# Kernel optimization log

Hardware: AMD Instinct MI355X
Metric: run time of the kernel (lower is better)

The kernel has to match this reference:

```python
import jax, jax.numpy as jnp
import numpy as np

N_NODES = 100000
N_EDGES = 1600000
IN_DIM, HID_DIM, OUT_DIM = 128, 256, 128


def gcn_conv(x, edge_index, W, b):
    """PyG GCNConv: add self-loops, sym-normalize, linear transform, scatter-add, bias."""
    n = x.shape[0]
    loop = jnp.arange(n, dtype=edge_index.dtype)
    src = jnp.concatenate([edge_index[0], loop])  # message source (x_j)
    dst = jnp.concatenate([edge_index[1], loop])  # aggregation target
    deg = jax.ops.segment_sum(jnp.ones_like(dst, dtype=x.dtype), dst, num_segments=n)
    dinv = jnp.where(deg > 0, deg ** -0.5, 0.0).astype(x.dtype)
    norm = dinv[src] * dinv[dst]                  # [E+N]
    h = x @ W                                     # [N, out]
    msg = h[src] * norm[:, None]                  # [E+N, out] gather
    out = jax.ops.segment_sum(msg, dst, num_segments=n)  # scatter-add
    return out + b


def setup_inputs() -> dict:
    key = jax.random.key(0)
    k = jax.random.split(key, 6)
    x = jax.random.normal(k[0], (N_NODES, IN_DIM), dtype=jnp.float32)
    edge_index = jax.random.randint(k[1], (2, N_EDGES), 0, N_NODES, dtype=jnp.int64)
    # Glorot-ish init for weights
    W1 = jax.random.normal(k[2], (IN_DIM, HID_DIM), dtype=jnp.float32) * (1.0 / np.sqrt(IN_DIM))
    b1 = jnp.zeros((HID_DIM,), dtype=jnp.float32)
    W2 = jax.random.normal(k[3], (HID_DIM, OUT_DIM), dtype=jnp.float32) * (1.0 / np.sqrt(HID_DIM))
    b2 = jnp.zeros((OUT_DIM,), dtype=jnp.float32)
    return {"x": x, "edge_index": edge_index, "W1": W1, "b1": b1, "W2": W2, "b2": b2}


def reference(x, edge_index, W1, b1, W2, b2):
    h = gcn_conv(x, edge_index, W1, b1)
    h = jax.nn.relu(h)  # relu between layers (drop_rate=0 -> no dropout)
    h = gcn_conv(h, edge_index, W2, b2)
    return h
```

## Files before the change

kernel.cpp:

```cpp
#include <hip/hip_runtime.h>
#include <hip/hip_bf16.h>

#define N_NODES 100000
#define N_EDGES 1600000
#define IN_DIM 128
#define HID_DIM 256
#define OUT_DIM 128
#define NB ((N_NODES + 1023) / 1024)
#define DCHUNK 12500
#define EGRID 8192
#define CAP 64
#define NSTRIP (N_NODES / 16)
#define GWAVES 2048

#define PB_ZERO 391
#define PB_E32  3125
#define PB_PREP 258
#define PB_CONVX 12500
#define PB_TOTAL (PB_ZERO + PB_E32 + PB_PREP + PB_CONVX)

typedef __attribute__((ext_vector_type(8))) short bf16x8;
typedef __attribute__((ext_vector_type(4))) float f32x4;
typedef __attribute__((ext_vector_type(4))) float float4v;
typedef unsigned long long ull;
typedef unsigned short u16;

__device__ __forceinline__ float bf2f(u16 u) {
  union { unsigned int i; float f; } c; c.i = ((unsigned int)u) << 16; return c.f;
}
__device__ __forceinline__ u16 f2bf(float f) {
  __hip_bfloat16 h = __float2bfloat16(f);
  return *(u16*)&h;
}

__global__ void detect_kernel(const int* __restrict__ ei,
                              const unsigned int* __restrict__ xw,
                              int* __restrict__ flags) {
  int lane = threadIdx.x;
  const long long* p = (const long long*)ei;
  long long v = p[lane & 15];
  int ebad = (lane < 16) && (v < 0 || v >= N_NODES);
  ull ebm = __ballot(ebad);
  int isf32 = 0;
  #pragma unroll
  for (int i = 0; i < 4; ++i) {
    unsigned int ex = (xw[lane * 4 + i] >> 7) & 0xFF;
    if (ex >= 0xC0) isf32 = 1;
  }
  ull fbm = __ballot(isf32);
  if (lane == 0) {
    flags[0] = (ebm == 0) ? 1 : 0;
    flags[1] = (fbm != 0) ? 1 : 0;
  }
}

__global__ void prologue_kernel(const int* __restrict__ ei, const void* __restrict__ x,
                                const void* __restrict__ W1, const void* __restrict__ b1,
                                const void* __restrict__ W2, const void* __restrict__ b2,
                                const int* __restrict__ flags,
                                int* __restrict__ deg, int* __restrict__ e32,
                                u16* __restrict__ Wt1, u16* __restrict__ Wt2,
                                u16* __restrict__ b1c, u16* __restrict__ b2c,
                                u16* __restrict__ xc) {
  int b = blockIdx.x, tid = threadIdx.x;
  if (b < PB_ZERO) {
    int i = b * 256 + tid;
    if (i < N_NODES) deg[i] = 0;
  } else if (b < PB_ZERO + PB_E32) {
    int i = (b - PB_ZERO) * 256 + tid;
    if (flags[0]) {
      const longlong2* p = (const longlong2*)ei;
      longlong2 v0 = p[i * 2], v1 = p[i * 2 + 1];
      ((int4*)e32)[i] = make_int4((int)v0.x, (int)v0.y, (int)v1.x, (int)v1.y);
    } else {
      ((int4*)e32)[i] = ((const int4*)ei)[i];
    }
  } else if (b < PB_ZERO + PB_E32 + PB_PREP) {
    int i = (b - PB_ZERO - PB_E32) * 256 + tid;
    int f = flags[1];
    auto cvt = [&](const void* P, int idx) -> u16 {
      return f ? f2bf(((const float*)P)[idx]) : ((const u16*)P)[idx];
    };
    if (i < 32768) {
      int k = i >> 8, n = i & 255;
      Wt1[n * 128 + k] = cvt(W1, i);
    } else if (i < 65536) {
      int j = i - 32768;
      int k = j >> 7, n = j & 127;
      Wt2[n * 256 + k] = cvt(W2, j);
    } else if (i < 65792) {
      b1c[i - 65536] = cvt(b1, i - 65536);
    } else if (i < 65920) {
      b2c[i - 65792] = cvt(b2, i - 65792);
    }
  } else {
    int i = (b - PB_ZERO - PB_E32 - PB_PREP) * 256 + tid;
    if (i >= N_NODES * IN_DIM / 4) return;
    if (flags[1]) {
      float4v v = ((const float4v*)x)[i];
      ull w = (ull)f2bf(v.x) | ((ull)f2bf(v.y) << 16) | ((ull)f2bf(v.z) << 32) |
              ((ull)f2bf(v.w) << 48);
      ((ull*)xc)[i] = w;
    } else {
      ((ull*)xc)[i] = ((const ull*)x)[i];
    }
  }
}

__global__ void fill_fixed_kernel(const int* __restrict__ esrc,
                                  const int* __restrict__ edst,
                                  int* __restrict__ cnt, int* __restrict__ csrf) {
  int g = blockIdx.x & 7;
  unsigned lo = (unsigned)(g * DCHUNK);
  unsigned hi = lo + DCHUNK; if (hi > N_NODES) hi = N_NODES;
  int stride = (EGRID >> 3) * 256;
  for (int e = (blockIdx.x >> 3) * 256 + threadIdx.x; e < N_EDGES; e += stride) {
    unsigned d = (unsigned)edst[e];
    if (d >= lo && d < hi) {
      int s = esrc[e];
      int p = atomicAdd(&cnt[d], 1);
      if (p < CAP) csrf[d * CAP + p] = s;
    }
  }
}

__global__ void degnorm_kernel(const int* __restrict__ cnt, float* __restrict__ dinv) {
  int i = blockIdx.x * 256 + threadIdx.x;
  if (i < N_NODES) dinv[i] = rsqrtf((float)(cnt[i] + 1));
}

__global__ void count_kernel(const int* __restrict__ edst, int* __restrict__ deg) {
  int g = blockIdx.x & 7;
  unsigned lo = (unsigned)(g * DCHUNK);
  unsigned hi = lo + DCHUNK; if (hi > N_NODES) hi = N_NODES;
  int stride = (EGRID >> 3) * 256;
  for (int e = (blockIdx.x >> 3) * 256 + threadIdx.x; e < N_EDGES; e += stride) {
    unsigned d = (unsigned)edst[e];
    if (d >= lo && d < hi) atomicAdd(&deg[d], 1);
  }
}

__global__ __launch_bounds__(1024) void bsum_kernel(const int* __restrict__ deg,
                                                    int* __restrict__ bsum, int n) {
  __shared__ int ws[16];
  int tid = threadIdx.x, lane = tid & 63, wid = tid >> 6;
  int idx = blockIdx.x * 1024 + tid;
  int v = (idx < n) ? deg[idx] : 0;
  #pragma unroll
  for (int o = 32; o > 0; o >>= 1) v += __shfl_down(v, o);
  if (lane == 0) ws[wid] = v;
  __syncthreads();
  if (tid == 0) {
    int r = 0;
    #pragma unroll
    for (int i = 0; i < 16; ++i) r += ws[i];
    bsum[blockIdx.x] = r;
  }
}

__global__ void bscan_kernel(const int* __restrict__ bsum, int* __restrict__ boff,
                             int* __restrict__ total, int nb) {
  int lane = threadIdx.x;
  int carry = 0;
  for (int c = 0; c < (nb + 63) / 64; ++c) {
    int idx = c * 64 + lane;
    int v = (idx < nb) ? bsum[idx] : 0;
    int x = v;
    #pragma unroll
    for (int o = 1; o < 64; o <<= 1) {
      int y = __shfl_up(x, o);
      if (lane >= o) x += y;
    }
    if (idx < nb) boff[idx] = carry + x - v;
    carry += __shfl(x, 63);
  }
  if (lane == 0) *total = carry;
}

__global__ __launch_bounds__(1024) void bfill_kernel(const int* __restrict__ deg,
                                                     const int* __restrict__ boff,
                                                     int* __restrict__ off,
                                                     int* __restrict__ cur,
                                                     float* __restrict__ dinv, int n) {
  __shared__ int wsum[16];
  __shared__ int wpre[16];
  int tid = threadIdx.x, lane = tid & 63, wid = tid >> 6;
  int idx = blockIdx.x * 1024 + tid;
  int v = (idx < n) ? deg[idx] : 0;
  int x = v;
  #pragma unroll
  for (int o = 1; o < 64; o <<= 1) {
    int y = __shfl_up(x, o);
    if (lane >= o) x += y;
  }
  if (lane == 63) wsum[wid] = x;
  __syncthreads();
  if (tid == 0) {
    int r = 0;
    #pragma unroll
    for (int i = 0; i < 16; ++i) { wpre[i] = r; r += wsum[i]; }
  }
  __syncthreads();
  int excl = boff[blockIdx.x] + wpre[wid] + x - v;
  if (idx < n) {
    off[idx] = excl;
    cur[idx] = excl;
    dinv[idx] = rsqrtf((float)(v + 1));
  }
}

__global__ void fill_kernel(const int* __restrict__ esrc, const int* __restrict__ edst,
                            int* __restrict__ cur, int* __restrict__ csr) {
  int g = blockIdx.x & 7;
  unsigned lo = (unsigned)(g * DCHUNK);
  unsigned hi = lo + DCHUNK; if (hi > N_NODES) hi = N_NODES;
  int stride = (EGRID >> 3) * 256;
  for (int e = (blockIdx.x >> 3) * 256 + threadIdx.x; e < N_EDGES; e += stride) {
    unsigned d = (unsigned)edst[e];
    if (d >= lo && d < hi) {
      int s = esrc[e];
      int p = atomicAdd(&cur[d], 1);
      if ((unsigned)p < N_EDGES) csr[p] = s;
    }
  }
}

template <bool BIAS, bool OUTF32, bool FIXED>
__global__ __launch_bounds__(256) void agg_kernel(
    const u16* __restrict__ V, const int* __restrict__ off,
    const int* __restrict__ csr, const float* __restrict__ dinv,
    const u16* __restrict__ bias, void* __restrict__ outv) {
  int d = (blockIdx.x * 256 + threadIdx.x) >> 6;
  int lane = threadIdx.x & 63;
  if (d >= N_NODES) return;
  int du = __builtin_amdgcn_readfirstlane(d);
  int grp = lane >> 4, sub = lane & 15;
  float dv = dinv[du];
  bf16x8 w0 = *(const bf16x8*)(V + (size_t)du * 128 + sub * 8);
  float self_s = (grp == 0) ? dv : 0.0f;
  float a[8];
  #pragma unroll
  for (int k = 0; k < 8; ++k) a[k] = self_s * bf2f((u16)w0[k]);
  int e, e1;
  if (FIXED) {
    int c = __builtin_amdgcn_readfirstlane(off[du]);
    if (c > CAP) c = CAP;
    e = du * CAP;
    e1 = e + c;
  } else {
    e  = __builtin_amdgcn_readfirstlane(off[du]);
    e1 = __builtin_amdgcn_readfirstlane(off[du + 1]);
  }
  for (; e + 8 <= e1; e += 8) {
    int sA = csr[e + grp];
    int sB = csr[e + 4 + grp];
    float dsA = dinv[sA];
    float dsB = dinv[sB];
    bf16x8 wA = *(const bf16x8*)(V + (size_t)sA * 128 + sub * 8);
    bf16x8 wB = *(const bf16x8*)(V + (size_t)sB * 128 + sub * 8);
    #pragma unroll
    for (int k = 0; k < 8; ++k) a[k] = fmaf(dsA, bf2f((u16)wA[k]), a[k]);
    #pragma unroll
    for (int k = 0; k < 8; ++k) a[k] = fmaf(dsB, bf2f((u16)wB[k]), a[k]);
  }
  for (; e + 4 <= e1; e += 4) {
    int s = csr[e + grp];
    float ds = dinv[s];
    bf16x8 w = *(const bf16x8*)(V + (size_t)s * 128 + sub * 8);
    #pragma unroll
    for (int k = 0; k < 8; ++k) a[k] = fmaf(ds, bf2f((u16)w[k]), a[k]);
  }
  int rem = e1 - e;
  if (rem > 0) {
    int ee = e + (grp < rem ? grp : 0);
    int s = csr[ee];
    float ds = (grp < rem) ? dinv[s] : 0.0f;
    bf16x8 w = *(const bf16x8*)(V + (size_t)s * 128 + sub * 8);
    #pragma unroll
    for (int k = 0; k < 8; ++k) a[k] = fmaf(ds, bf2f((u16)w[k]), a[k]);
  }
  #pragma unroll
  for (int k = 0; k < 8; ++k) {
    a[k] += __shfl_xor(a[k], 16);
    a[k] += __shfl_xor(a[k], 32);
    a[k] *= dv;
  }
  if (BIAS) {
    bf16x8 bv = *(const bf16x8*)(bias + sub * 8);
    #pragma unroll
    for (int k = 0; k < 8; ++k) a[k] += bf2f((u16)bv[k]);
  }
  if (OUTF32) {
    if (grp < 2) {
      f32x4 o4;
      #pragma unroll
      for (int r = 0; r < 4; ++r) o4[r] = a[grp * 4 + r];
      *(f32x4*)((float*)outv + (size_t)du * 128 + sub * 8 + grp * 4) = o4;
    }
  } else {
    if (grp == 0) {
      bf16x8 ob;
      #pragma unroll
      for (int k = 0; k < 8; ++k) ob[k] = (short)f2bf(a[k]);
      *(bf16x8*)((u16*)outv + (size_t)du * 128 + sub * 8) = ob;
    }
  }
}

__global__ __launch_bounds__(256) void mlp1_kernel(
    const u16* __restrict__ xa, const u16* __restrict__ Wt1,
    const u16* __restrict__ b1, u16* __restrict__ h) {
  __shared__ u16 B[32768];
  int tid = threadIdx.x;
  #pragma unroll
  for (int j = 0; j < 16; ++j) {
    int i = j * 256 + tid;
    int row = i >> 4, blk = i & 15;
    int phys = (row << 4) | (blk ^ (row & 15));
    *(bf16x8*)&B[phys * 8] = *(const bf16x8*)(Wt1 + (size_t)i * 8);
  }
  __syncthreads();
  int wid = tid >> 6, lane = tid & 63, ml = lane & 15, q = lane >> 4;
  for (int s = blockIdx.x * 4 + wid; s < NSTRIP; s += GWAVES) {
    const short* Ar = (const short*)xa + (size_t)(s * 16 + ml) * IN_DIM + q * 8;
    f32x4 acc[16] = {};
    #pragma unroll
    for (int k0 = 0; k0 < IN_DIM; k0 += 32) {
      bf16x8 a = *(const bf16x8*)(Ar + k0);
      int kb = k0 >> 3;
      #pragma unroll
      for (int t = 0; t < 16; ++t) {
        int brow = t * 16 + ml;
        const u16* Bp = &B[(((unsigned)brow << 4) | (unsigned)((kb + q) ^ ml)) * 8];
        acc[t] = __builtin_amdgcn_mfma_f32_16x16x32_bf16(a, *(const bf16x8*)Bp, acc[t], 0, 0, 0);
      }
    }
    size_t hb = (size_t)s * 16 * HID_DIM;
    #pragma unroll
    for (int t = 0; t < 16; ++t) {
      float bv = bf2f(b1[t * 16 + ml]);
      #pragma unroll
      for (int r = 0; r < 4; ++r)
        h[hb + (size_t)(q * 4 + r) * HID_DIM + t * 16 + ml] =
            f2bf(fmaxf(acc[t][r] + bv, 0.0f));
    }
  }
}

__global__ __launch_bounds__(256) void mlp2_kernel(
    const u16* __restrict__ h, const u16* __restrict__ Wt2, u16* __restrict__ xg) {
  __shared__ u16 B[32768];
  int tid = threadIdx.x;
  #pragma unroll
  for (int j = 0; j < 16; ++j) {
    int i = j * 256 + tid;
    int row = i >> 5, blk = i & 31;
    int phys = (row << 5) | (blk ^ (row & 15));
    *(bf16x8*)&B[phys * 8] = *(const bf16x8*)(Wt2 + (size_t)i * 8);
  }
  __syncthreads();
  int wid = tid >> 6, lane = tid & 63, ml = lane & 15, q = lane >> 4;
  for (int s = blockIdx.x * 4 + wid; s < NSTRIP; s += GWAVES) {
    const short* Ar = (const short*)h + (size_t)(s * 16 + ml) * HID_DIM + q * 8;
    f32x4 acc[8] = {};
    #pragma unroll
    for (int k0 = 0; k0 < HID_DIM; k0 += 32) {
      bf16x8 a = *(const bf16x8*)(Ar + k0);
      int kb = k0 >> 3;
      #pragma unroll
      for (int t = 0; t < 8; ++t) {
        int brow = t * 16 + ml;
        const u16* Bp = &B[(((unsigned)brow << 5) | (unsigned)((kb + q) ^ ml)) * 8];
        acc[t] = __builtin_amdgcn_mfma_f32_16x16x32_bf16(a, *(const bf16x8*)Bp, acc[t], 0, 0, 0);
      }
    }
    size_t gb = (size_t)s * 16 * OUT_DIM;
    #pragma unroll
    for (int t = 0; t < 8; ++t) {
      #pragma unroll
      for (int r = 0; r < 4; ++r)
        xg[gb + (size_t)(q * 4 + r) * OUT_DIM + t * 16 + ml] = f2bf(acc[t][r]);
    }
  }
}

extern "C" void kernel_launch(void* const* d_in, const int* in_sizes, int n_in,
                              void* d_out, int out_size, void* d_ws, size_t ws_size,
                              hipStream_t stream) {
  const void* x  = d_in[0];
  const int*  ei = (const int*)d_in[1];
  const void* W1 = d_in[2];
  const void* b1 = d_in[3];
  const void* W2 = d_in[4];
  const void* b2 = d_in[5];

  char* wsb = (char*)d_ws;

  {
    size_t o = 0;
    auto carve = [&](size_t bytes) {
      o = (o + 511) & ~(size_t)511;
      void* p = wsb + o;
      o += bytes;
      return p;
    };
    int*   flags = (int*)carve(8);
    int*   cnt  = (int*)carve((size_t)N_NODES * 4);
    float* dinv = (float*)carve((size_t)N_NODES * 4);
    int*   csrf = (int*)carve((size_t)N_NODES * CAP * 4);
    u16*   Wt1 = (u16*)carve((size_t)IN_DIM * HID_DIM * 2);
    u16*   Wt2 = (u16*)carve((size_t)HID_DIM * OUT_DIM * 2);
    u16*   b1c = (u16*)carve((size_t)HID_DIM * 2);
    u16*   b2c = (u16*)carve((size_t)OUT_DIM * 2);
    u16*   xc  = (u16*)carve((size_t)N_NODES * 128 * 2);
    u16*   xa  = (u16*)carve((size_t)N_NODES * 128 * 2);
    u16*   h   = (u16*)d_out;
    int*   e32 = (int*)xa;
    int*   esrc = e32;
    int*   edst = e32 + N_EDGES;
    if (o <= ws_size) {
      detect_kernel<<<1, 64, 0, stream>>>(ei, (const unsigned int*)x, flags);
      prologue_kernel<<<PB_TOTAL, 256, 0, stream>>>(ei, x, W1, b1, W2, b2, flags,
                                                    cnt, e32, Wt1, Wt2, b1c, b2c, xc);
      fill_fixed_kernel<<<EGRID, 256, 0, stream>>>(esrc, edst, cnt, csrf);
      degnorm_kernel<<<(N_NODES + 255) / 256, 256, 0, stream>>>(cnt, dinv);
      agg_kernel<false, false, true>
          <<<(N_NODES * 64) / 256, 256, 0, stream>>>(xc, cnt, csrf, dinv, nullptr, xa);
      mlp1_kernel<<<512, 256, 0, stream>>>(xa, Wt1, b1c, h);
      mlp2_kernel<<<512, 256, 0, stream>>>(h, Wt2, xa);
      agg_kernel<true, true, true>
          <<<(N_NODES * 64) / 256, 256, 0, stream>>>(xa, cnt, csrf, dinv, b2c, d_out);
      return;
    }
  }

  size_t o = 0;
  auto carve = [&](size_t bytes) {
    o = (o + 511) & ~(size_t)511;
    void* p = wsb + o;
    o += bytes;
    return p;
  };
  int*   flags = (int*)carve(8);
  int*   deg  = (int*)carve((size_t)N_NODES * 4);
  int*   off  = (int*)carve((size_t)(N_NODES + 1) * 4);
  int*   cur  = (int*)carve((size_t)N_NODES * 4);
  float* dinv = (float*)carve((size_t)N_NODES * 4);
  int*   csr  = (int*)carve((size_t)N_EDGES * 4);
  int*   bsum = (int*)carve((size_t)NB * 4);
  int*   boff = (int*)carve((size_t)NB * 4);
  u16*   Wt1 = (u16*)carve((size_t)IN_DIM * HID_DIM * 2);
  u16*   Wt2 = (u16*)carve((size_t)HID_DIM * OUT_DIM * 2);
  u16*   b1c = (u16*)carve((size_t)HID_DIM * 2);
  u16*   b2c = (u16*)carve((size_t)OUT_DIM * 2);
  u16*   xc  = (u16*)carve((size_t)N_NODES * 128 * 2);
  u16*   xa  = (u16*)carve((size_t)N_NODES * 128 * 2);
  u16*   h   = (u16*)d_out;
  int*   e32 = (int*)xa;
  int*   esrc = e32;
  int*   edst = e32 + N_EDGES;

  detect_kernel<<<1, 64, 0, stream>>>(ei, (const unsigned int*)x, flags);
  prologue_kernel<<<PB_TOTAL, 256, 0, stream>>>(ei, x, W1, b1, W2, b2, flags,
                                                deg, e32, Wt1, Wt2, b1c, b2c, xc);
  count_kernel<<<EGRID, 256, 0, stream>>>(edst, deg);
  bsum_kernel<<<NB, 1024, 0, stream>>>(deg, bsum, N_NODES);
  bscan_kernel<<<1, 64, 0, stream>>>(bsum, boff, off + N_NODES, NB);
  bfill_kernel<<<NB, 1024, 0, stream>>>(deg, boff, off, cur, dinv, N_NODES);
  fill_kernel<<<EGRID, 256, 0, stream>>>(esrc, edst, cur, csr);

  agg_kernel<false, false, false>
      <<<(N_NODES * 64) / 256, 256, 0, stream>>>(xc, off, csr, dinv, nullptr, xa);
  mlp1_kernel<<<512, 256, 0, stream>>>(xa, Wt1, b1c, h);
  mlp2_kernel<<<512, 256, 0, stream>>>(h, Wt2, xa);
  agg_kernel<true, true, false>
      <<<(N_NODES * 64) / 256, 256, 0, stream>>>(xa, off, csr, dinv, b2c, d_out);
}
```

Before: 357.0 us.

## Read int64 edge indices directly in fill kernels, drop int32 conversion pass

Removes the prologue stage that narrowed the int64 edge_index into a temporary int32 buffer; the count, fill and fixed-capacity fill kernels now read the original edge array directly, choosing the dtype at runtime. The fixed-capacity fill is also rewritten so each thread handles 8 consecutive edges with vector loads and one pass over all destinations, replacing the 8-way destination-range partitioned grid-stride loop that rescanned the edge list eight times. This cuts one full write and read of the edge list and most of the redundant destination reads. In exchange, the atomics now hit all destinations at once and lose the locality the range partitioning gave.

```diff
diff --git a/kernel.cpp b/kernel.cpp
--- a/kernel.cpp
+++ b/kernel.cpp
@@ -10,14 +10,14 @@
 #define DCHUNK 12500
 #define EGRID 8192
 #define CAP 64
+#define FFGRID 782
 #define NSTRIP (N_NODES / 16)
 #define GWAVES 2048
 
 #define PB_ZERO 391
-#define PB_E32  3125
 #define PB_PREP 258
 #define PB_CONVX 12500
-#define PB_TOTAL (PB_ZERO + PB_E32 + PB_PREP + PB_CONVX)
+#define PB_TOTAL (PB_ZERO + PB_PREP + PB_CONVX)
 
 typedef __attribute__((ext_vector_type(8))) short bf16x8;
 typedef __attribute__((ext_vector_type(4))) float f32x4;
@@ -54,29 +54,24 @@
   }
 }
 
-__global__ void prologue_kernel(const int* __restrict__ ei, const void* __restrict__ x,
+__device__ __forceinline__ int edge_at(const int* ei, int idx, int mode) {
+  return mode ? (int)((const long long*)ei)[idx] : ei[idx];
+}
+
+__global__ void prologue_kernel(const void* __restrict__ x,
                                 const void* __restrict__ W1, const void* __restrict__ b1,
                                 const void* __restrict__ W2, const void* __restrict__ b2,
                                 const int* __restrict__ flags,
-                                int* __restrict__ deg, int* __restrict__ e32,
+                                int* __restrict__ cnt,
                                 u16* __restrict__ Wt1, u16* __restrict__ Wt2,
                                 u16* __restrict__ b1c, u16* __restrict__ b2c,
                                 u16* __restrict__ xc) {
   int b = blockIdx.x, tid = threadIdx.x;
   if (b < PB_ZERO) {
     int i = b * 256 + tid;
-    if (i < N_NODES) deg[i] = 0;
-  } else if (b < PB_ZERO + PB_E32) {
+    if (i < N_NODES) cnt[i] = 0;
+  } else if (b < PB_ZERO + PB_PREP) {
     int i = (b - PB_ZERO) * 256 + tid;
-    if (flags[0]) {
-      const longlong2* p = (const longlong2*)ei;
-      longlong2 v0 = p[i * 2], v1 = p[i * 2 + 1];
-      ((int4*)e32)[i] = make_int4((int)v0.x, (int)v0.y, (int)v1.x, (int)v1.y);
-    } else {
-      ((int4*)e32)[i] = ((const int4*)ei)[i];
-    }
-  } else if (b < PB_ZERO + PB_E32 + PB_PREP) {
-    int i = (b - PB_ZERO - PB_E32) * 256 + tid;
     int f = flags[1];
     auto cvt = [&](const void* P, int idx) -> u16 {
       return f ? f2bf(((const float*)P)[idx]) : ((const u16*)P)[idx];
@@ -94,7 +89,7 @@
       b2c[i - 65792] = cvt(b2, i - 65792);
     }
   } else {
-    int i = (b - PB_ZERO - PB_E32 - PB_PREP) * 256 + tid;
+    int i = (b - PB_ZERO - PB_PREP) * 256 + tid;
     if (i >= N_NODES * IN_DIM / 4) return;
     if (flags[1]) {
       float4v v = ((const float4v*)x)[i];
@@ -107,37 +102,61 @@
   }
 }
 
-__global__ void fill_fixed_kernel(const int* __restrict__ esrc,
-                                  const int* __restrict__ edst,
+__global__ void fill_fixed_kernel(const int* __restrict__ ei,
+                                  const int* __restrict__ flags,
                                   int* __restrict__ cnt, int* __restrict__ csrf) {
+  int tg = blockIdx.x * 256 + threadIdx.x;
+  int base = tg * 8;
+  if (base >= N_EDGES) return;
+  int dv[8], sv[8];
+  if (flags[0]) {
+    const longlong2* ps = (const longlong2*)ei + (base >> 1);
+    const longlong2* pd = (const longlong2*)ei + ((N_EDGES + base) >> 1);
+    #pragma unroll
+    for (int k = 0; k < 4; ++k) {
+      longlong2 s2 = ps[k], d2 = pd[k];
+      sv[2 * k] = (int)s2.x; sv[2 * k + 1] = (int)s2.y;
+      dv[2 * k] = (int)d2.x; dv[2 * k + 1] = (int)d2.y;
+    }
+  } else {
+    int4 s0 = *(const int4*)(ei + base);
+    int4 s1 = *(const int4*)(ei + base + 4);
+    int4 d0 = *(const int4*)(ei + N_EDGES + base);
+    int4 d1 = *(const int4*)(ei + N_EDGES + base + 4);
+    sv[0] = s0.x; sv[1] = s0.y; sv[2] = s0.z; sv[3] = s0.w;
+    sv[4] = s1.x; sv[5] = s1.y; sv[6] = s1.z; sv[7] = s1.w;
+    dv[0] = d0.x; dv[1] = d0.y; dv[2] = d0.z; dv[3] = d0.w;
+    dv[4] = d1.x; dv[5] = d1.y; dv[6] = d1.z; dv[7] = d1.w;
+  }
+  int p8[8];
+  #pragma unroll
+  for (int k = 0; k < 8; ++k) p8[k] = atomicAdd(&cnt[dv[k]], 1);
+  #pragma unroll
+  for (int k = 0; k < 8; ++k)
+    if (p8[k] < CAP) csrf[dv[k] * CAP + p8[k]] = sv[k];
+}
+
+__global__ void degnorm_kernel(const int* __restrict__ cnt, float* __restrict__ dinv) {
+  int i = blockIdx.x * 256 + threadIdx.x;
+  if (i < N_NODES) dinv[i] = rsqrtf((float)(cnt[i] + 1));
+}
+
+__global__ void count_kernel(const int* __restrict__ ei, const int* __restrict__ flags,
+                             int* __restrict__ deg) {
   int g = blockIdx.x & 7;
   unsigned lo = (unsigned)(g * DCHUNK);
   unsigned hi = lo + DCHUNK; if (hi > N_NODES) hi = N_NODES;
+  int m = flags[0];
   int stride = (EGRID >> 3) * 256;
   for (int e = (blockIdx.x >> 3) * 256 + threadIdx.x; e < N_EDGES; e += stride) {
-    unsigned d = (unsigned)edst[e];
-    if (d >= lo && d < hi) {
-      int s = esrc[e];
-      int p = atomicAdd(&cnt[d], 1);
-      if (p < CAP) csrf[d * CAP + p] = s;
-    }
-  }
-}
-
-__global__ void degnorm_kernel(const int* __restrict__ cnt, float* __restrict__ dinv) {
+    unsigned d = (unsigned)edge_at(ei, N_EDGES + e, m);
+    if (d >= lo && d < hi) atomicAdd(&deg[d], 1);
+  }
+}
+
+__global__ void zero_kernel(int* p, int n) {
   int i = blockIdx.x * 256 + threadIdx.x;
-  if (i < N_NODES) dinv[i] = rsqrtf((float)(cnt[i] + 1));
-}
-
-__global__ void count_kernel(const int* __restrict__ edst, int* __restrict__ deg) {
-  int g = blockIdx.x & 7;
-  unsigned lo = (unsigned)(g * DCHUNK);
-  unsigned hi = lo + DCHUNK; if (hi > N_NODES) hi = N_NODES;
-  int stride = (EGRID >> 3) * 256;
-  for (int e = (blockIdx.x >> 3) * 256 + threadIdx.x; e < N_EDGES; e += stride) {
-    unsigned d = (unsigned)edst[e];
-    if (d >= lo && d < hi) atomicAdd(&deg[d], 1);
-  }
+  if (i < n) p[i] = 0;
 }
 
 __global__ __launch_bounds__(1024) void bsum_kernel(const int* __restrict__ deg,
@@ -209,16 +228,17 @@
   }
 }
 
-__global__ void fill_kernel(const int* __restrict__ esrc, const int* __restrict__ edst,
+__global__ void fill_kernel(const int* __restrict__ ei, const int* __restrict__ flags,
                             int* __restrict__ cur, int* __restrict__ csr) {
   int g = blockIdx.x & 7;
   unsigned lo = (unsigned)(g * DCHUNK);
   unsigned hi = lo + DCHUNK; if (hi > N_NODES) hi = N_NODES;
+  int m = flags[0];
   int stride = (EGRID >> 3) * 256;
   for (int e = (blockIdx.x >> 3) * 256 + threadIdx.x; e < N_EDGES; e += stride) {
-    unsigned d = (unsigned)edst[e];
+    unsigned d = (unsigned)edge_at(ei, N_EDGES + e, m);
     if (d >= lo && d < hi) {
-      int s = esrc[e];
+      int s = edge_at(ei, e, m);
       int p = atomicAdd(&cur[d], 1);
       if ((unsigned)p < N_EDGES) csr[p] = s;
     }
@@ -415,14 +435,11 @@
     u16*   xc  = (u16*)carve((size_t)N_NODES * 128 * 2);
     u16*   xa  = (u16*)carve((size_t)N_NODES * 128 * 2);
     u16*   h   = (u16*)d_out;
-    int*   e32 = (int*)xa;
-    int*   esrc = e32;
-    int*   edst = e32 + N_EDGES;
     if (o <= ws_size) {
       detect_kernel<<<1, 64, 0, stream>>>(ei, (const unsigned int*)x, flags);
-      prologue_kernel<<<PB_TOTAL, 256, 0, stream>>>(ei, x, W1, b1, W2, b2, flags,
-                                                    cnt, e32, Wt1, Wt2, b1c, b2c, xc);
-      fill_fixed_kernel<<<EGRID, 256, 0, stream>>>(esrc, edst, cnt, csrf);
+      prologue_kernel<<<PB_TOTAL, 256, 0, stream>>>(x, W1, b1, W2, b2, flags,
+                                                    cnt, Wt1, Wt2, b1c, b2c, xc);
+      fill_fixed_kernel<<<FFGRID, 256, 0, stream>>>(ei, flags, cnt, csrf);
       degnorm_kernel<<<(N_NODES + 255) / 256, 256, 0, stream>>>(cnt, dinv);
       agg_kernel<false, false, true>
           <<<(N_NODES * 64) / 256, 256, 0, stream>>>(xc, cnt, csrf, dinv, nullptr, xa);
@@ -456,18 +473,16 @@
   u16*   xc  = (u16*)carve((size_t)N_NODES * 128 * 2);
   u16*   xa  = (u16*)carve((size_t)N_NODES * 128 * 2);
   u16*   h   = (u16*)d_out;
-  int*   e32 = (int*)xa;
-  int*   esrc = e32;
-  int*   edst = e32 + N_EDGES;
 
   detect_kernel<<<1, 64, 0, stream>>>(ei, (const unsigned int*)x, flags);
-  prologue_kernel<<<PB_TOTAL, 256, 0, stream>>>(ei, x, W1, b1, W2, b2, flags,
-                                                deg, e32, Wt1, Wt2, b1c, b2c, xc);
-  count_kernel<<<EGRID, 256, 0, stream>>>(edst, deg);
+  zero_kernel<<<(N_NODES + 255) / 256, 256, 0, stream>>>(deg, N_NODES);
+  prologue_kernel<<<PB_TOTAL, 256, 0, stream>>>(x, W1, b1, W2, b2, flags,
+                                                deg, Wt1, Wt2, b1c, b2c, xc);
+  count_kernel<<<EGRID, 256, 0, stream>>>(ei, flags, deg);
   bsum_kernel<<<NB, 1024, 0, stream>>>(deg, bsum, N_NODES);
   bscan_kernel<<<1, 64, 0, stream>>>(bsum, boff, off + N_NODES, NB);
   bfill_kernel<<<NB, 1024, 0, stream>>>(deg, boff, off, cur, dinv, N_NODES);
-  fill_kernel<<<EGRID, 256, 0, stream>>>(esrc, edst, cur, csr);
+  fill_kernel<<<EGRID, 256, 0, stream>>>(ei, flags, cur, csr);
 
   agg_kernel<false, false, false>
       <<<(N_NODES * 64) / 256, 256, 0, stream>>>(xc, off, csr, dinv, nullptr, xa);
```

After: 414.0 us. 16.0% more time.
